# Performance work log

Hardware: AMD Instinct MI355X
Metric: run time of the kernel (lower is better)

## Reference

```python
import jax, jax.numpy as jnp
import numpy as np

FA, FB_CAT, FM, HID = 133, 147, 8, 100  # atom feat, bond feat (concat), mol feat, hidden
N_ATOMS, N_BONDS, N_MOLS, MAX_NB = 250000, 500000, 10000, 6
DEPTH = 3


def setup_inputs() -> dict:
    key = jax.random.key(0)
    ks = jax.random.split(key, 10)
    f_atoms = jax.random.normal(ks[0], (N_ATOMS, FA), jnp.float32)
    f_bonds = jax.random.normal(ks[1], (N_BONDS, FB_CAT), jnp.float32)
    f_mol = jax.random.normal(ks[2], (N_MOLS, FM), jnp.float32)
    a2b = jax.random.randint(ks[3], (N_ATOMS, MAX_NB), 0, N_BONDS, jnp.int32)
    b2a = jax.random.randint(ks[4], (N_BONDS,), 0, N_ATOMS, jnp.int32)
    b2revb = jax.random.randint(ks[5], (N_BONDS,), 0, N_BONDS, jnp.int32)
    # contiguous molecules of 25 atoms each -> equivalent of ascope segments
    mol_id = (jnp.arange(N_ATOMS, dtype=jnp.int32) // (N_ATOMS // N_MOLS))
    # parameters (Linear with bias=False): stored as (in, out)
    W_i = jax.random.normal(ks[6], (FB_CAT, HID), jnp.float32) * 0.05
    W_h = jax.random.normal(ks[7], (HID, HID), jnp.float32) * 0.05
    W_o = jax.random.normal(ks[8], (HID + FA, HID), jnp.float32) * 0.05
    return {"f_atoms": f_atoms, "f_bonds": f_bonds, "f_mol": f_mol,
            "W_i": W_i, "W_h": W_h, "W_o": W_o,
            "a2b": a2b, "b2a": b2a, "b2revb": b2revb,
            "mol_id": mol_id, "n_mols": N_MOLS}


def reference(f_atoms, f_bonds, f_mol, W_i, W_h, W_o, a2b, b2a, b2revb, mol_id, n_mols):
    act = jax.nn.relu
    inp = act(f_bonds @ W_i)              # (B, H)
    message = inp
    for _ in range(DEPTH - 1):
        nei = message[a2b]                # (A, MAX_NB, H) gather
        a_message = nei.sum(axis=1)       # (A, H)
        message = a_message[b2a] - message[b2revb]  # (B, H)
        message = act(inp + message @ W_h)
        # dropout p=0 (eval) -> identity
    # readout to atoms
    a_message = message[a2b].sum(axis=1)  # (A, H)
    a_input = jnp.concatenate([f_atoms, a_message], axis=1)  # (A, FA+H)
    atom_hiddens = act(a_input @ W_o)     # (A, H)
    # per-molecule mean over ragged segments (ascope equivalent)
    mol_sum = jax.ops.segment_sum(atom_hiddens, mol_id, num_segments=n_mols)
    counts = jax.ops.segment_sum(jnp.ones((atom_hiddens.shape[0],), atom_hiddens.dtype),
                                 mol_id, num_segments=n_mols)
    mol_vecs = mol_sum / jnp.maximum(counts, 1.0)[:, None]  # zero-vec for empty mols
    mol_vecs = jnp.concatenate([mol_vecs, f_mol], axis=1)   # (M, H+FM)
    return mol_vecs, atom_hiddens
```

## Files before the change

kernel.cpp:

```cpp
#include <hip/hip_runtime.h>

#define THREADS 256
#define MS 128

typedef __bf16 bf16x8 __attribute__((ext_vector_type(8)));
typedef float f32x4 __attribute__((ext_vector_type(4)));
typedef float f32x4u __attribute__((ext_vector_type(4), aligned(4)));

__device__ __forceinline__ unsigned short f2b(float x) {
    unsigned int u = __float_as_uint(x);
    u = (u + 0x7FFFu + ((u >> 16) & 1u)) >> 16;
    return (unsigned short)u;
}
__device__ __forceinline__ float b2f(unsigned short h) {
    return __uint_as_float(((unsigned int)h) << 16);
}
__device__ __forceinline__ bf16x8 as_bf(uint4 q) {
    union { uint4 q; bf16x8 v; } u; u.q = q; return u.v;
}

__device__ __forceinline__ void pack_body(const float* __restrict__ W,
                                          unsigned short* __restrict__ out,
                                          int K, int bid, int l)
{
    int kc = bid / 7, nt = bid - kc * 7;
    int k0 = kc * 32 + (l >> 4) * 8;
    int n = nt * 16 + (l & 15);
    unsigned short v[8];
    #pragma unroll
    for (int j = 0; j < 8; ++j) {
        int k = k0 + j;
        float x = (k < K && n < 100) ? W[(size_t)k * 100 + n] : 0.f;
        v[j] = f2b(x);
    }
    *(uint4*)&out[((size_t)bid * 64 + l) * 8] = *(uint4*)v;
}

__device__ __forceinline__ void pack_wo_body(const float* __restrict__ W,
                                             unsigned short* __restrict__ out,
                                             int bid, int l)
{
    int kc = bid / 7, nt = bid - kc * 7;
    int k0 = kc * 32 + (l >> 4) * 8;
    int n = nt * 16 + (l & 15);
    unsigned short v[8];
    #pragma unroll
    for (int j = 0; j < 8; ++j) {
        int k = k0 + j;
        float x = 0.f;
        if (n < 100) {
            if (k < 100)                  x = W[(size_t)(133 + k) * 100 + n];
            else if (k >= 112 && k < 245) x = W[(size_t)(k - 112) * 100 + n];
        }
        v[j] = f2b(x);
    }
    *(uint4*)&out[((size_t)bid * 64 + l) * 8] = *(uint4*)v;
}

__global__ __launch_bounds__(64) void prep(
    const float* __restrict__ Wi, const float* __restrict__ Wh, const float* __restrict__ Wo,
    unsigned short* __restrict__ wfi, unsigned short* __restrict__ wfh,
    unsigned short* __restrict__ wfo, float* __restrict__ out_mol, int nmol_floats)
{
    int bid = blockIdx.x;
    int l = threadIdx.x;
    if (bid < 35) {
        pack_body(Wi, wfi, 147, bid, l);
    } else if (bid < 63) {
        pack_body(Wh, wfh, 100, bid - 35, l);
    } else if (bid < 119) {
        pack_wo_body(Wo, wfo, bid - 63, l);
    } else {
        int idx = (bid - 119) * 64 + l;
        int stride = (gridDim.x - 119) * 64;
        for (int i = idx; i * 4 < nmol_floats; i += stride)
            *(f32x4*)&out_mol[(size_t)i * 4] = (f32x4){0.f, 0.f, 0.f, 0.f};
    }
}

__global__ __launch_bounds__(THREADS) void gather_sum_bf16(
    const unsigned short* __restrict__ msg, const int* __restrict__ a2b,
    unsigned short* __restrict__ amsg, int A)
{
    int t = blockIdx.x * THREADS + threadIdx.x;
    if (t >= A * 16) return;
    int a = t >> 4;
    int c = t & 15;
    if (c >= 14) {
        *(uint4*)&amsg[(size_t)a * MS + c * 8] = make_uint4(0u, 0u, 0u, 0u);
        return;
    }
    const int* nb = a2b + (size_t)a * 6;
    float s[8];
    #pragma unroll
    for (int e = 0; e < 8; ++e) s[e] = 0.f;
    #pragma unroll
    for (int j = 0; j < 6; ++j) {
        uint4 v = *(const uint4*)&msg[(size_t)nb[j] * MS + c * 8];
        const unsigned short* pv = (const unsigned short*)&v;
        #pragma unroll
        for (int e = 0; e < 8; ++e) s[e] += b2f(pv[e]);
    }
    unsigned short r[8];
    #pragma unroll
    for (int e = 0; e < 8; ++e) r[e] = f2b(s[e]);
    *(uint4*)&amsg[(size_t)a * MS + c * 8] = *(uint4*)r;
}

__global__ __launch_bounds__(THREADS) void gemm_in(
    const float* __restrict__ fb, const unsigned short* __restrict__ wf,
    unsigned short* __restrict__ Y, int M)
{
    constexpr int KS = 168;
    __shared__ char smem[64 * KS * 2];
    unsigned short* Xs = (unsigned short*)smem;
    unsigned short* Os = (unsigned short*)smem;

    const int tid = threadIdx.x;
    const int l = tid & 63, w = tid >> 6;
    const int quad = l >> 4, c15 = l & 15;
    const int row0 = blockIdx.x * 64;

    for (int t = tid; t < 64 * 20; t += THREADS) {
        int rl = t / 20, c = t - rl * 20;
        int rr = min(row0 + rl, M - 1);
        const float* rowp = fb + (size_t)rr * 147 + c * 8;
        unsigned short tt[8];
        if (c < 18) {
            f32x4u x0 = *(const f32x4u*)(rowp);
            f32x4u x1 = *(const f32x4u*)(rowp + 4);
            #pragma unroll
            for (int e = 0; e < 4; ++e) { tt[e] = f2b(x0[e]); tt[4 + e] = f2b(x1[e]); }
        } else if (c == 18) {
            #pragma unroll
            for (int j = 0; j < 8; ++j)
                tt[j] = (j < 3) ? f2b(rowp[j]) : (unsigned short)0;
        } else {
            #pragma unroll
            for (int j = 0; j < 8; ++j) tt[j] = 0;
        }
        *(uint4*)&Xs[(size_t)rl * KS + c * 8] = *(uint4*)tt;
    }
    __syncthreads();

    f32x4 acc[7];
    #pragma unroll
    for (int nt = 0; nt < 7; ++nt) acc[nt] = (f32x4){0.f, 0.f, 0.f, 0.f};
    const unsigned short* xrow = Xs + (size_t)(w * 16 + c15) * KS + quad * 8;
    #pragma unroll
    for (int kc = 0; kc < 5; ++kc) {
        bf16x8 av = *(const bf16x8*)(xrow + kc * 32);
        #pragma unroll
        for (int nt = 0; nt < 7; ++nt) {
            uint4 bq = *(const uint4*)&wf[((size_t)(kc * 7 + nt) * 64 + l) * 8];
            acc[nt] = __builtin_amdgcn_mfma_f32_16x16x32_bf16(av, as_bf(bq), acc[nt], 0, 0, 0);
        }
    }
    __syncthreads();

    #pragma unroll
    for (int nt = 0; nt < 7; ++nt)
        #pragma unroll
        for (int reg = 0; reg < 4; ++reg)
            Os[(w * 16 + quad * 4 + reg) * 136 + nt * 16 + c15] = f2b(fmaxf(acc[nt][reg], 0.f));
    __syncthreads();

    for (int t = tid; t < 64 * 16; t += THREADS) {
        int rl = t >> 4, c = t & 15;
        int rr = row0 + rl;
        if (rr < M) {
            uint4 o = (c < 14) ? *(const uint4*)&Os[rl * 136 + c * 8]
                               : make_uint4(0u, 0u, 0u, 0u);
            *(uint4*)&Y[(size_t)rr * MS + c * 8] = o;
        }
    }
}

__global__ __launch_bounds__(THREADS) void gemm_msg(
    const unsigned short* __restrict__ amsg, const unsigned short* __restrict__ msg,
    const int* __restrict__ b2a, const int* __restrict__ b2revb,
    const unsigned short* __restrict__ wf, const unsigned short* __restrict__ bias,
    unsigned short* __restrict__ Y, int M, int last)
{
    __shared__ unsigned short Os[64 * 136];
    const int tid = threadIdx.x;
    const int l = tid & 63, w = tid >> 6;
    const int quad = l >> 4, c15 = l & 15;
    const int row0 = blockIdx.x * 64;
    const int rc = min(row0 + w * 16 + c15, M - 1);
    const int iA = b2a[rc], iB = b2revb[rc];
    const unsigned short* pa = amsg + (size_t)iA * MS + quad * 8;
    const unsigned short* pb = msg  + (size_t)iB * MS + quad * 8;

    uint4 a1[4], a2[4];
    #pragma unroll
    for (int kc = 0; kc < 4; ++kc) {
        a1[kc] = *(const uint4*)(pa + kc * 32);
        a2[kc] = *(const uint4*)(pb + kc * 32);
    }

    f32x4 acc1[7], acc2[7];
    #pragma unroll
    for (int nt = 0; nt < 7; ++nt) {
        acc1[nt] = (f32x4){0.f, 0.f, 0.f, 0.f};
        acc2[nt] = (f32x4){0.f, 0.f, 0.f, 0.f};
    }
    #pragma unroll
    for (int kc = 0; kc < 4; ++kc) {
        #pragma unroll
        for (int nt = 0; nt < 7; ++nt) {
            uint4 bq = *(const uint4*)&wf[((size_t)(kc * 7 + nt) * 64 + l) * 8];
            acc1[nt] = __builtin_amdgcn_mfma_f32_16x16x32_bf16(as_bf(a1[kc]), as_bf(bq), acc1[nt], 0, 0, 0);
            acc2[nt] = __builtin_amdgcn_mfma_f32_16x16x32_bf16(as_bf(a2[kc]), as_bf(bq), acc2[nt], 0, 0, 0);
        }
    }

    #pragma unroll
    for (int nt = 0; nt < 7; ++nt)
        #pragma unroll
        for (int reg = 0; reg < 4; ++reg)
            Os[(w * 16 + quad * 4 + reg) * 136 + nt * 16 + c15] = f2b(acc1[nt][reg] - acc2[nt][reg]);
    __syncthreads();

    for (int t = tid; t < 64 * 16; t += THREADS) {
        int rl = t >> 4, c = t & 15;
        int rr = row0 + rl;
        if (rr >= M) continue;
        if (c < 14) {
            uint4 o = *(const uint4*)&Os[rl * 136 + c * 8];
            uint4 bq = *(const uint4*)&bias[(size_t)rr * MS + c * 8];
            const unsigned short* po = (const unsigned short*)&o;
            const unsigned short* pq = (const unsigned short*)&bq;
            unsigned short res[8];
            #pragma unroll
            for (int e = 0; e < 8; ++e)
                res[e] = f2b(fmaxf(b2f(po[e]) + b2f(pq[e]), 0.f));
            *(uint4*)&Y[(size_t)rr * MS + c * 8] = *(uint4*)res;
        } else if (!last) {
            *(uint4*)&Y[(size_t)rr * MS + c * 8] = make_uint4(0u, 0u, 0u, 0u);
        }
    }
}

__global__ __launch_bounds__(THREADS) void gemm_out(
    const float* __restrict__ fa, const unsigned short* __restrict__ msg,
    const int* __restrict__ a2b, const unsigned short* __restrict__ wf,
    const int* __restrict__ mol_id, float* __restrict__ Y,
    float* __restrict__ out_mol, int M)
{
    constexpr int KS = 264;
    __shared__ char smem[64 * KS * 2];
    __shared__ int mids[64];
    unsigned short* Xs = (unsigned short*)smem;
    float* Os = (float*)smem;

    const int tid = threadIdx.x;
    const int l = tid & 63, w = tid >> 6;
    const int quad = l >> 4, c15 = l & 15;
    const int row0 = blockIdx.x * 64;

    if (tid < 64) {
        int rr = row0 + tid;
        mids[tid] = (rr < M) ? mol_id[rr] : -1;
    }

    for (int t = tid; t < 64 * 33; t += THREADS) {
        int rl = t / 33, c = t - rl * 33;
        int rr = min(row0 + rl, M - 1);
        uint4 o;
        if (c < 14) {
            const int* nb = a2b + (size_t)rr * 6;
            float s[8];
            #pragma unroll
            for (int e = 0; e < 8; ++e) s[e] = 0.f;
            #pragma unroll
            for (int j = 0; j < 6; ++j) {
                uint4 v = *(const uint4*)&msg[(size_t)nb[j] * MS + c * 8];
                const unsigned short* pv = (const unsigned short*)&v;
                #pragma unroll
                for (int e = 0; e < 8; ++e) s[e] += b2f(pv[e]);
            }
            unsigned short r[8];
            #pragma unroll
            for (int e = 0; e < 8; ++e) r[e] = f2b(s[e]);
            o = *(uint4*)r;
        } else if (c < 30) {
            int cc = c - 14;
            f32x4u x0 = *(const f32x4u*)(fa + (size_t)rr * 133 + cc * 8);
            f32x4u x1 = *(const f32x4u*)(fa + (size_t)rr * 133 + cc * 8 + 4);
            unsigned short tt[8];
            #pragma unroll
            for (int e = 0; e < 4; ++e) { tt[e] = f2b(x0[e]); tt[4 + e] = f2b(x1[e]); }
            o = *(uint4*)tt;
        } else if (c == 30) {
            unsigned short tt[8];
            #pragma unroll
            for (int j = 0; j < 8; ++j) {
                int col = 128 + j;
                tt[j] = (col < 133) ? f2b(fa[(size_t)rr * 133 + col]) : (unsigned short)0;
            }
            o = *(uint4*)tt;
        } else {
            o = make_uint4(0u, 0u, 0u, 0u);
        }
        *(uint4*)&Xs[(size_t)rl * KS + c * 8] = o;
    }
    __syncthreads();

    f32x4 acc[7];
    #pragma unroll
    for (int nt = 0; nt < 7; ++nt) acc[nt] = (f32x4){0.f, 0.f, 0.f, 0.f};
    const unsigned short* xrow = Xs + (size_t)(w * 16 + c15) * KS + quad * 8;
    #pragma unroll
    for (int kc = 0; kc < 8; ++kc) {
        bf16x8 av = *(const bf16x8*)(xrow + kc * 32);
        #pragma unroll
        for (int nt = 0; nt < 7; ++nt) {
            uint4 bq = *(const uint4*)&wf[((size_t)(kc * 7 + nt) * 64 + l) * 8];
            acc[nt] = __builtin_amdgcn_mfma_f32_16x16x32_bf16(av, as_bf(bq), acc[nt], 0, 0, 0);
        }
    }
    __syncthreads();

    #pragma unroll
    for (int nt = 0; nt < 7; ++nt) {
        int n = nt * 16 + c15;
        if (n < 100) {
            #pragma unroll
            for (int reg = 0; reg < 4; ++reg)
                Os[(w * 16 + quad * 4 + reg) * 108 + n] = fmaxf(acc[nt][reg], 0.f);
        }
    }
    __syncthreads();

    for (int t = tid; t < 64 * 25; t += THREADS) {
        int rl = t / 25, c = t - rl * 25;
        int rr = row0 + rl;
        if (rr < M)
            *(f32x4*)&Y[(size_t)rr * 100 + c * 4] = *(const f32x4*)&Os[rl * 108 + c * 4];
    }

    if (tid < 100) {
        int c = tid;
        float s = 0.f;
        int cur = mids[0];
        #pragma unroll 1
        for (int rl = 0; rl < 64; ++rl) {
            int mid = mids[rl];
            if (mid != cur) {
                if (cur >= 0) atomicAdd(&out_mol[(size_t)cur * 108 + c], s);
                s = 0.f;
                cur = mid;
            }
            if (mid < 0) break;
            s += Os[rl * 108 + c];
        }
        if (cur >= 0) atomicAdd(&out_mol[(size_t)cur * 108 + c], s);
    }
}

__global__ __launch_bounds__(128) void finalize(
    float* __restrict__ out_mol, const float* __restrict__ f_mol,
    const int* __restrict__ mol_id, int n_atoms)
{
    int m = blockIdx.x;
    int lo = 0, hi = n_atoms;
    while (lo < hi) { int mid = (lo + hi) >> 1; if (mol_id[mid] < m) lo = mid + 1; else hi = mid; }
    int lo2 = lo, hi2 = n_atoms;
    while (lo2 < hi2) { int mid = (lo2 + hi2) >> 1; if (mol_id[mid] < m + 1) lo2 = mid + 1; else hi2 = mid; }
    float inv = 1.0f / fmaxf((float)(lo2 - lo), 1.0f);
    int c = threadIdx.x;
    if (c < 100) {
        out_mol[(size_t)m * 108 + c] *= inv;
    } else if (c < 108) {
        out_mol[(size_t)m * 108 + c] = f_mol[(size_t)m * 8 + (c - 100)];
    }
}

extern "C" void kernel_launch(void* const* d_in, const int* in_sizes, int n_in,
                              void* d_out, int out_size, void* d_ws, size_t ws_size,
                              hipStream_t stream)
{
    const float* f_atoms = (const float*)d_in[0];
    const float* f_bonds = (const float*)d_in[1];
    const float* f_mol   = (const float*)d_in[2];
    const float* W_i     = (const float*)d_in[3];
    const float* W_h     = (const float*)d_in[4];
    const float* W_o     = (const float*)d_in[5];
    const int* a2b    = (const int*)d_in[6];
    const int* b2a    = (const int*)d_in[7];
    const int* b2revb = (const int*)d_in[8];
    const int* mol_id = (const int*)d_in[9];

    const int A    = in_sizes[0] / 133;
    const int B    = in_sizes[1] / 147;
    const int Mmol = in_sizes[2] / 8;

    unsigned short* wsu = (unsigned short*)d_ws;
    unsigned short* wfi  = wsu;
    unsigned short* wfh  = wfi + 35 * 512;
    unsigned short* wfo  = wfh + 28 * 512;
    unsigned short* amsg = wfo + 56 * 512;
    unsigned short* inp  = amsg + (size_t)A * MS;
    unsigned short* msgA = inp  + (size_t)B * MS;
    unsigned short* msgB = msgA + (size_t)B * MS;

    float* out     = (float*)d_out;
    float* out_mol = out;
    float* atom_h  = out + (size_t)Mmol * 108;

    dim3 blk(THREADS);
    int gB = (B + 63) / 64;
    int gA = (A + 63) / 64;
    int gg = (A * 16 + THREADS - 1) / THREADS;

    prep<<<119 + 256, dim3(64), 0, stream>>>(W_i, W_h, W_o, wfi, wfh, wfo,
                                             out_mol, Mmol * 108);

    gemm_in<<<gB, blk, 0, stream>>>(f_bonds, wfi, inp, B);

    gather_sum_bf16<<<gg, blk, 0, stream>>>(inp, a2b, amsg, A);
    gemm_msg<<<gB, blk, 0, stream>>>(amsg, inp, b2a, b2revb, wfh, inp, msgA, B, 0);

    gather_sum_bf16<<<gg, blk, 0, stream>>>(msgA, a2b, amsg, A);
    gemm_msg<<<gB, blk, 0, stream>>>(amsg, msgA, b2a, b2revb, wfh, inp, msgB, B, 1);

    gemm_out<<<gA, blk, 0, stream>>>(f_atoms, msgB, a2b, wfo, mol_id, atom_h, out_mol, A);

    finalize<<<Mmol, dim3(128), 0, stream>>>(out_mol, f_mol, mol_id, A);
}
```

Baseline: 1.039 ms.

## Fuse neighbor gather-sum into message GEMM via swizzled LDS staging

Removes the separate per-atom gather_sum kernel and the amsg intermediate buffer. Each bond block now gathers and sums the six neighbor messages of its source atom directly, and stages that sum and the reverse-bond message in XOR-swizzled shared memory before the MFMA loop. This eliminates two launches and the amsg write/read round trip. In exchange, the atom gather is recomputed once per bond (about twice per atom), which raises random reads, and the larger shared buffer may reduce occupancy.

```diff
diff --git a/kernel.cpp b/kernel.cpp
--- a/kernel.cpp
+++ b/kernel.cpp
@@ -78,35 +78,6 @@
     }
 }
 
-__global__ __launch_bounds__(THREADS) void gather_sum_bf16(
-    const unsigned short* __restrict__ msg, const int* __restrict__ a2b,
-    unsigned short* __restrict__ amsg, int A)
-{
-    int t = blockIdx.x * THREADS + threadIdx.x;
-    if (t >= A * 16) return;
-    int a = t >> 4;
-    int c = t & 15;
-    if (c >= 14) {
-        *(uint4*)&amsg[(size_t)a * MS + c * 8] = make_uint4(0u, 0u, 0u, 0u);
-        return;
-    }
-    const int* nb = a2b + (size_t)a * 6;
-    float s[8];
-    #pragma unroll
-    for (int e = 0; e < 8; ++e) s[e] = 0.f;
-    #pragma unroll
-    for (int j = 0; j < 6; ++j) {
-        uint4 v = *(const uint4*)&msg[(size_t)nb[j] * MS + c * 8];
-        const unsigned short* pv = (const unsigned short*)&v;
-        #pragma unroll
-        for (int e = 0; e < 8; ++e) s[e] += b2f(pv[e]);
-    }
-    unsigned short r[8];
-    #pragma unroll
-    for (int e = 0; e < 8; ++e) r[e] = f2b(s[e]);
-    *(uint4*)&amsg[(size_t)a * MS + c * 8] = *(uint4*)r;
-}
-
 __global__ __launch_bounds__(THREADS) void gemm_in(
     const float* __restrict__ fb, const unsigned short* __restrict__ wf,
     unsigned short* __restrict__ Y, int M)
@@ -176,28 +147,49 @@
     }
 }
 
-__global__ __launch_bounds__(THREADS) void gemm_msg(
-    const unsigned short* __restrict__ amsg, const unsigned short* __restrict__ msg,
+__global__ __launch_bounds__(THREADS) void gemm_msg_f(
+    const unsigned short* __restrict__ msg, const int* __restrict__ a2b,
     const int* __restrict__ b2a, const int* __restrict__ b2revb,
     const unsigned short* __restrict__ wf, const unsigned short* __restrict__ bias,
     unsigned short* __restrict__ Y, int M, int last)
 {
-    __shared__ unsigned short Os[64 * 136];
+    __shared__ char smem[64 * 256 * 2];
+    unsigned short* As = (unsigned short*)smem;
+    unsigned short* Bs = (unsigned short*)(smem + 64 * 256);
+    unsigned short* Os = (unsigned short*)smem;
+
     const int tid = threadIdx.x;
     const int l = tid & 63, w = tid >> 6;
     const int quad = l >> 4, c15 = l & 15;
     const int row0 = blockIdx.x * 64;
-    const int rc = min(row0 + w * 16 + c15, M - 1);
-    const int iA = b2a[rc], iB = b2revb[rc];
-    const unsigned short* pa = amsg + (size_t)iA * MS + quad * 8;
-    const unsigned short* pb = msg  + (size_t)iB * MS + quad * 8;
-
-    uint4 a1[4], a2[4];
-    #pragma unroll
-    for (int kc = 0; kc < 4; ++kc) {
-        a1[kc] = *(const uint4*)(pa + kc * 32);
-        a2[kc] = *(const uint4*)(pb + kc * 32);
-    }
+
+    for (int t = tid; t < 64 * 16; t += THREADS) {
+        int rl = t >> 4, c = t & 15;
+        int rr = min(row0 + rl, M - 1);
+        int sc = (c ^ (rl & 7)) * 8;
+        *(uint4*)&Bs[rl * 128 + sc] =
+            *(const uint4*)&msg[(size_t)b2revb[rr] * MS + c * 8];
+        uint4 o = make_uint4(0u, 0u, 0u, 0u);
+        if (c < 14) {
+            const int* nb = a2b + (size_t)b2a[rr] * 6;
+            float s[8];
+            #pragma unroll
+            for (int e = 0; e < 8; ++e) s[e] = 0.f;
+            #pragma unroll
+            for (int j = 0; j < 6; ++j) {
+                uint4 v = *(const uint4*)&msg[(size_t)nb[j] * MS + c * 8];
+                const unsigned short* pv = (const unsigned short*)&v;
+                #pragma unroll
+                for (int e = 0; e < 8; ++e) s[e] += b2f(pv[e]);
+            }
+            unsigned short r8[8];
+            #pragma unroll
+            for (int e = 0; e < 8; ++e) r8[e] = f2b(s[e]);
+            o = *(uint4*)r8;
+        }
+        *(uint4*)&As[rl * 128 + sc] = o;
+    }
+    __syncthreads();
 
     f32x4 acc1[7], acc2[7];
     #pragma unroll
@@ -205,15 +197,21 @@
         acc1[nt] = (f32x4){0.f, 0.f, 0.f, 0.f};
         acc2[nt] = (f32x4){0.f, 0.f, 0.f, 0.f};
     }
+    const int r = w * 16 + c15;
+    const int rx = r & 7;
     #pragma unroll
     for (int kc = 0; kc < 4; ++kc) {
+        int chk = ((kc * 4 + quad) ^ rx) * 8;
+        bf16x8 av = *(const bf16x8*)&As[r * 128 + chk];
+        bf16x8 bv = *(const bf16x8*)&Bs[r * 128 + chk];
         #pragma unroll
         for (int nt = 0; nt < 7; ++nt) {
             uint4 bq = *(const uint4*)&wf[((size_t)(kc * 7 + nt) * 64 + l) * 8];
-            acc1[nt] = __builtin_amdgcn_mfma_f32_16x16x32_bf16(as_bf(a1[kc]), as_bf(bq), acc1[nt], 0, 0, 0);
-            acc2[nt] = __builtin_amdgcn_mfma_f32_16x16x32_bf16(as_bf(a2[kc]), as_bf(bq), acc2[nt], 0, 0, 0);
-        }
-    }
+            acc1[nt] = __builtin_amdgcn_mfma_f32_16x16x32_bf16(av, as_bf(bq), acc1[nt], 0, 0, 0);
+            acc2[nt] = __builtin_amdgcn_mfma_f32_16x16x32_bf16(bv, as_bf(bq), acc2[nt], 0, 0, 0);
+        }
+    }
+    __syncthreads();
 
     #pragma unroll
     for (int nt = 0; nt < 7; ++nt)
@@ -400,8 +398,7 @@
     unsigned short* wfi  = wsu;
     unsigned short* wfh  = wfi + 35 * 512;
     unsigned short* wfo  = wfh + 28 * 512;
-    unsigned short* amsg = wfo + 56 * 512;
-    unsigned short* inp  = amsg + (size_t)A * MS;
+    unsigned short* inp  = wfo + 56 * 512;
     unsigned short* msgA = inp  + (size_t)B * MS;
     unsigned short* msgB = msgA + (size_t)B * MS;
 
@@ -412,18 +409,14 @@
     dim3 blk(THREADS);
     int gB = (B + 63) / 64;
     int gA = (A + 63) / 64;
-    int gg = (A * 16 + THREADS - 1) / THREADS;
 
     prep<<<119 + 256, dim3(64), 0, stream>>>(W_i, W_h, W_o, wfi, wfh, wfo,
                                              out_mol, Mmol * 108);
 
     gemm_in<<<gB, blk, 0, stream>>>(f_bonds, wfi, inp, B);
 
-    gather_sum_bf16<<<gg, blk, 0, stream>>>(inp, a2b, amsg, A);
-    gemm_msg<<<gB, blk, 0, stream>>>(amsg, inp, b2a, b2revb, wfh, inp, msgA, B, 0);
-
-    gather_sum_bf16<<<gg, blk, 0, stream>>>(msgA, a2b, amsg, A);
-    gemm_msg<<<gB, blk, 0, stream>>>(amsg, msgA, b2a, b2revb, wfh, inp, msgB, B, 1);
+    gemm_msg_f<<<gB, blk, 0, stream>>>(inp,  a2b, b2a, b2revb, wfh, inp, msgA, B, 0);
+    gemm_msg_f<<<gB, blk, 0, stream>>>(msgA, a2b, b2a, b2revb, wfh, inp, msgB, B, 1);
 
     gemm_out<<<gA, blk, 0, stream>>>(f_atoms, msgB, a2b, wfo, mol_id, atom_h, out_mol, A);
 
```

Result: slower. 1.106 ms (+6.4%).
